# Performance work log

Measured on AMD Instinct MI355X. Metric: run time of the kernel, lower is better.

## Reference

```python
import jax, jax.numpy as jnp
import numpy as np

D = 512
H = 8
HD = D // H  # 64
B = 16
N = 64        # seq_len (variable nodes)
S = N + 1     # new_seq (with CLS)
THRESHOLD = 0.5
LN_EPS = 1e-5


def setup_inputs() -> dict:
    key = jax.random.key(0)
    ks = jax.random.split(key, 12)
    s = 0.02
    return {
        "desc_embeddings": jax.random.normal(ks[0], (B, N, D), jnp.float32),
        "name_value_embeddings": jax.random.normal(ks[1], (B, S, D), jnp.float32),
        "w_gt": jax.random.normal(ks[2], (D, D), jnp.float32) * s,
        "b_gt": jnp.zeros((D,), jnp.float32),
        "topology_bias": jnp.zeros((1,), jnp.float32),
        "w_edge1": jax.random.normal(ks[3], (2 * D, D), jnp.float32) * s,
        "b_edge1": jnp.zeros((D,), jnp.float32),
        "ln_gamma": jnp.ones((D,), jnp.float32),
        "ln_beta": jnp.zeros((D,), jnp.float32),
        "w_edge2": jax.random.normal(ks[4], (D, D), jnp.float32) * s,
        "b_edge2": jnp.zeros((D,), jnp.float32),
        "w_q": jax.random.normal(ks[5], (D, D), jnp.float32) * s,
        "b_q": jnp.zeros((D,), jnp.float32),
        "w_k": jax.random.normal(ks[6], (D, D), jnp.float32) * s,
        "b_k": jnp.zeros((D,), jnp.float32),
        "w_v": jax.random.normal(ks[7], (D, D), jnp.float32) * s,
        "b_v": jnp.zeros((D,), jnp.float32),
        "w_attn": jax.random.normal(ks[8], (3 * HD,), jnp.float32) * s,
        "b_attn": jnp.zeros((1,), jnp.float32),
        "w_out": jax.random.normal(ks[9], (D, D), jnp.float32) * s,
        "b_out": jnp.zeros((D,), jnp.float32),
    }


def _layernorm(x, gamma, beta):
    mu = jnp.mean(x, axis=-1, keepdims=True)
    var = jnp.mean(jnp.square(x - mu), axis=-1, keepdims=True)
    return (x - mu) * jax.lax.rsqrt(var + LN_EPS) * gamma + beta


def reference(desc_embeddings, name_value_embeddings, w_gt, b_gt, topology_bias,
              w_edge1, b_edge1, ln_gamma, ln_beta, w_edge2, b_edge2,
              w_q, b_q, w_k, b_k, w_v, b_v, w_attn, b_attn, w_out, b_out):
    b, s, d = name_value_embeddings.shape
    n = s - 1

    # 1. Global topology (projected desc embeddings, cosine sim, sigmoid)
    de = desc_embeddings @ w_gt + b_gt                                   # [B,N,D]
    de_n = de / jnp.linalg.norm(de, axis=-1, keepdims=True)
    global_sim = jnp.einsum('bnd,bmd->bnm', de_n, de_n)
    gt = jax.nn.sigmoid(global_sim + topology_bias)
    # straight-through threshold (frozen=False)
    hard = (gt > THRESHOLD).astype(gt.dtype)
    gA = hard - jax.lax.stop_gradient(gt) + gt

    # 2. Sample-wise similarity over variable tokens
    var = name_value_embeddings[:, 1:, :]
    var_n = var / jnp.linalg.norm(var, axis=-1, keepdims=True)
    sample_sim = jnp.einsum('bnd,bmd->bnm', var_n, var_n)

    # no self-interaction, then graph-conditioned softmax
    gA = gA * (1.0 - jnp.eye(n, dtype=gt.dtype))[None]
    adjacency = jax.nn.softmax(gA * sample_sim, axis=-1)                 # [B,N,N]

    # 4. Edge attributes [B,S,S,2D] and padded adjacency [B,S,S]
    var_edge = jnp.concatenate([
        jnp.broadcast_to(de[:, :, None, :], (b, n, n, d)),
        jnp.broadcast_to(de[:, None, :, :], (b, n, n, d)),
    ], axis=-1)
    cls_edge = jnp.concatenate([de, de], axis=-1)                        # [B,N,2D]
    edge_attr = jnp.zeros((b, s, s, 2 * d), de.dtype)
    edge_attr = edge_attr.at[:, 1:, 1:].set(var_edge)
    edge_attr = edge_attr.at[:, 0, 1:].set(cls_edge)
    edge_attr = edge_attr.at[:, 1:, 0].set(cls_edge)

    new_adj = jnp.zeros((b, s, s), adjacency.dtype)
    new_adj = new_adj.at[:, 1:, 1:].set(adjacency)
    new_adj = new_adj.at[:, 0, 1:].set(1.0)

    # 5. Attention
    q = (name_value_embeddings @ w_q + b_q).reshape(b, s, H, HD).transpose(0, 2, 1, 3)
    k = (name_value_embeddings @ w_k + b_k).reshape(b, s, H, HD).transpose(0, 2, 1, 3)
    v = (name_value_embeddings @ w_v + b_v).reshape(b, s, H, HD).transpose(0, 2, 1, 3)

    # edge MLP: Linear -> LayerNorm -> ReLU -> Linear
    eu = jax.nn.relu(_layernorm(edge_attr @ w_edge1 + b_edge1, ln_gamma, ln_beta)) @ w_edge2 + b_edge2
    eu = eu.reshape(b, s, s, H, HD)                                      # [B,S,S,H,hd]

    # attn_proj(concat([q_i, k_j, e_ij])) decomposed into three dot products
    wq_a, wk_a, we_a = w_attn[:HD], w_attn[HD:2 * HD], w_attn[2 * HD:]
    score_q = jnp.einsum('bhid,d->bhi', q, wq_a)[:, :, :, None]
    score_k = jnp.einsum('bhjd,d->bhj', k, wk_a)[:, :, None, :]
    # edge features are pre-masked by adjacency; linearity lets us mask the score
    score_e = jnp.einsum('bijhd,d->bhij', eu, we_a) * new_adj[:, None]
    attn = score_q + score_k + score_e + b_attn[0]

    attn = attn + jnp.where(new_adj[:, None] == 0, -1e9, 0.0)
    attn = jax.nn.softmax(attn, axis=-1)                                 # [B,H,S,S]
    # dropout p=0 (eval)

    context = jnp.einsum('bhij,bhjd->bhid', attn, v)
    context = context.transpose(0, 2, 1, 3).reshape(b, s, d)
    output = context @ w_out + b_out
    return output, attn
```

## Files before the change

### kernel.cpp

```cpp
#include <hip/hip_runtime.h>
#include <math.h>


constexpr int kD  = 512;
constexpr int kH  = 8;
constexpr int kHD = 64;
constexpr int kB  = 16;
constexpr int kN  = 64;
constexpr int kS  = 65;

typedef short bf16x8 __attribute__((ext_vector_type(8)));
typedef float f32x4  __attribute__((ext_vector_type(4)));

__device__ __forceinline__ float wsum(float x) {
#pragma unroll
  for (int m = 1; m < 64; m <<= 1) x += __shfl_xor(x, m, 64);
  return x;
}
__device__ __forceinline__ float wmax(float x) {
#pragma unroll
  for (int m = 1; m < 64; m <<= 1) x = fmaxf(x, __shfl_xor(x, m, 64));
  return x;
}
__device__ __forceinline__ float osum(float x) {
  x += __shfl_xor(x, 8, 64);
  x += __shfl_xor(x, 16, 64);
  x += __shfl_xor(x, 32, 64);
  return x;
}

__device__ __forceinline__ unsigned short f2bf(float x) {
  unsigned int u = __builtin_bit_cast(unsigned int, x);
  u += 0x7FFFu + ((u >> 16) & 1u);
  return (unsigned short)(u >> 16);
}
__device__ __forceinline__ float bf2f(unsigned short h) {
  return __builtin_bit_cast(float, ((unsigned int)h) << 16);
}
__device__ __forceinline__ unsigned int pk2(unsigned short a, unsigned short b) {
  return (unsigned int)a | ((unsigned int)b << 16);
}

__global__ __launch_bounds__(256) void conv_w(
    const float* __restrict__ w_q, const float* __restrict__ w_k,
    const float* __restrict__ w_v, const float* __restrict__ w_e1,
    const float* __restrict__ w_o, unsigned short* __restrict__ wt)
{
  __shared__ float T[32][33];
  const int z = blockIdx.z;
  const float* src = (z == 0) ? w_q : (z == 1) ? w_k : (z == 2) ? w_v
                   : (z == 3) ? w_e1 : (z == 4) ? (w_e1 + 262144) : w_o;
  unsigned short* hi = wt + (size_t)z * 524288;
  unsigned short* lo = hi + 262144;
  const int n0 = blockIdx.x * 32, k0 = blockIdx.y * 32;
  const int tx = threadIdx.x & 31, ty0 = threadIdx.x >> 5;
#pragma unroll
  for (int it = 0; it < 4; ++it) {
    const int ky = ty0 + it * 8;
    T[ky][tx] = src[(size_t)(k0 + ky) * kD + n0 + tx];
  }
  __syncthreads();
#pragma unroll
  for (int it = 0; it < 4; ++it) {
    const int ny = ty0 + it * 8;
    const float x = T[tx][ny];
    const unsigned short h = f2bf(x);
    hi[(size_t)(n0 + ny) * kD + k0 + tx] = h;
    lo[(size_t)(n0 + ny) * kD + k0 + tx] = f2bf(x - bf2f(h));
  }
}

__global__ __launch_bounds__(256) void gemm_f32(
    const float* __restrict__ A, const float* __restrict__ W,
    const float* __restrict__ bias, float* __restrict__ C)
{
  __shared__ float Ast[32][65];
  __shared__ float Bs[32][68];
  const int bm = blockIdx.x * 64, bn = blockIdx.y * 64;
  const int tid = threadIdx.x;
  const int ar = tid >> 2, ak = (tid & 3) * 8;
  const int bkr = tid >> 3, bn0 = (tid & 7) * 8;
  const int tx = tid & 15, ty = tid >> 4;
  const float* Ap = A + (size_t)(bm + ar) * kD + ak;
  const float* Wp = W + (size_t)bkr * kD + bn + bn0;

  float4 a0 = *reinterpret_cast<const float4*>(Ap);
  float4 a1 = *reinterpret_cast<const float4*>(Ap + 4);
  float4 b0 = *reinterpret_cast<const float4*>(Wp);
  float4 b1 = *reinterpret_cast<const float4*>(Wp + 4);

  float acc[4][4] = {};
  for (int kt = 0; kt < 16; ++kt) {
    Ast[ak + 0][ar] = a0.x; Ast[ak + 1][ar] = a0.y;
    Ast[ak + 2][ar] = a0.z; Ast[ak + 3][ar] = a0.w;
    Ast[ak + 4][ar] = a1.x; Ast[ak + 5][ar] = a1.y;
    Ast[ak + 6][ar] = a1.z; Ast[ak + 7][ar] = a1.w;
    *reinterpret_cast<float4*>(&Bs[bkr][bn0])     = b0;
    *reinterpret_cast<float4*>(&Bs[bkr][bn0 + 4]) = b1;
    __syncthreads();
    if (kt + 1 < 16) {
      const float* Ap2 = Ap + (kt + 1) * 32;
      const float* Wp2 = Wp + (size_t)(kt + 1) * 32 * kD;
      a0 = *reinterpret_cast<const float4*>(Ap2);
      a1 = *reinterpret_cast<const float4*>(Ap2 + 4);
      b0 = *reinterpret_cast<const float4*>(Wp2);
      b1 = *reinterpret_cast<const float4*>(Wp2 + 4);
    }
#pragma unroll
    for (int kk = 0; kk < 32; ++kk) {
      const float x0 = Ast[kk][ty * 4 + 0];
      const float x1 = Ast[kk][ty * 4 + 1];
      const float x2 = Ast[kk][ty * 4 + 2];
      const float x3 = Ast[kk][ty * 4 + 3];
      const float4 bv = *reinterpret_cast<const float4*>(&Bs[kk][tx * 4]);
      acc[0][0] = fmaf(x0, bv.x, acc[0][0]); acc[0][1] = fmaf(x0, bv.y, acc[0][1]);
      acc[0][2] = fmaf(x0, bv.z, acc[0][2]); acc[0][3] = fmaf(x0, bv.w, acc[0][3]);
      acc[1][0] = fmaf(x1, bv.x, acc[1][0]); acc[1][1] = fmaf(x1, bv.y, acc[1][1]);
      acc[1][2] = fmaf(x1, bv.z, acc[1][2]); acc[1][3] = fmaf(x1, bv.w, acc[1][3]);
      acc[2][0] = fmaf(x2, bv.x, acc[2][0]); acc[2][1] = fmaf(x2, bv.y, acc[2][1]);
      acc[2][2] = fmaf(x2, bv.z, acc[2][2]); acc[2][3] = fmaf(x2, bv.w, acc[2][3]);
      acc[3][0] = fmaf(x3, bv.x, acc[3][0]); acc[3][1] = fmaf(x3, bv.y, acc[3][1]);
      acc[3][2] = fmaf(x3, bv.z, acc[3][2]); acc[3][3] = fmaf(x3, bv.w, acc[3][3]);
    }
    __syncthreads();
  }
#pragma unroll
  for (int i = 0; i < 4; ++i) {
    const int row = bm + ty * 4 + i;
#pragma unroll
    for (int j = 0; j < 4; ++j) {
      const int col = bn + tx * 4 + j;
      C[(size_t)row * kD + col] = acc[i][j] + bias[col];
    }
  }
}

struct MJob { const float* A; const unsigned short* Wh; const unsigned short* Wl;
              const float* bias; float* C; int M; };
struct MJobs { MJob j[3]; };

__global__ __launch_bounds__(256) void gemm_mfma(
    MJobs jobs, int zNorms,
    const float* __restrict__ deN, const float* __restrict__ nvN,
    float* __restrict__ invde, float* __restrict__ invvar)
{
  if ((int)blockIdx.z == zNorms) {
    const int flat = blockIdx.x + gridDim.x * blockIdx.y;
    const int lane = threadIdx.x & 63;
    const int w = threadIdx.x >> 6;
#pragma unroll
    for (int r = 0; r < 4; ++r) {
      const int wid = flat * 16 + w * 4 + r;
      if (wid >= 2 * kB * kN) break;
      const float* row;
      if (wid < kB * kN) {
        row = deN + (size_t)wid * kD;
      } else {
        const int t = wid - kB * kN;
        row = nvN + ((size_t)(t / kN) * kS + 1 + (t % kN)) * kD;
      }
      const float4* r4 = reinterpret_cast<const float4*>(row) + lane * 2;
      const float4 x0 = r4[0], x1 = r4[1];
      float ss = x0.x * x0.x + x0.y * x0.y + x0.z * x0.z + x0.w * x0.w
               + x1.x * x1.x + x1.y * x1.y + x1.z * x1.z + x1.w * x1.w;
      ss = wsum(ss);
      if (lane == 0) {
        const float inv = 1.f / sqrtf(ss);
        if (wid < kB * kN) invde[wid] = inv; else invvar[wid - kB * kN] = inv;
      }
    }
    return;
  }

  const MJob jb = jobs.j[blockIdx.z];
  __shared__ unsigned short Ah[64][40], Al[64][40], Wh[64][40], Wl[64][40];
  const int tid = threadIdx.x;
  const int lane = tid & 63, wv = tid >> 6;
  const int wr = wv >> 1, wc = wv & 1;
  const int bm = blockIdx.x * 64, bn = blockIdx.y * 64;
  const int sr = tid >> 2, sk = (tid & 3) * 8;
  const bool aok = (bm + sr) < jb.M;
  const float* Ap = jb.A + (size_t)(bm + sr) * kD + sk;
  const unsigned short* Whp = jb.Wh + (size_t)(bn + sr) * kD + sk;
  const unsigned short* Wlp = jb.Wl + (size_t)(bn + sr) * kD + sk;

  const f32x4 zero = {0.f, 0.f, 0.f, 0.f};
  f32x4 acc00 = zero, acc01 = zero, acc10 = zero, acc11 = zero;

  for (int k0 = 0; k0 < kD; k0 += 32) {
    float4 a0 = {0.f, 0.f, 0.f, 0.f}, a1 = {0.f, 0.f, 0.f, 0.f};
    if (aok) {
      a0 = *reinterpret_cast<const float4*>(Ap + k0);
      a1 = *reinterpret_cast<const float4*>(Ap + k0 + 4);
    }
    const uint4 wh4 = *reinterpret_cast<const uint4*>(Whp + k0);
    const uint4 wl4 = *reinterpret_cast<const uint4*>(Wlp + k0);
    const float av[8] = {a0.x, a0.y, a0.z, a0.w, a1.x, a1.y, a1.z, a1.w};
    unsigned short h[8], l[8];
#pragma unroll
    for (int e = 0; e < 8; ++e) {
      h[e] = f2bf(av[e]);
      l[e] = f2bf(av[e] - bf2f(h[e]));
    }
    const uint4 hp = { pk2(h[0], h[1]), pk2(h[2], h[3]), pk2(h[4], h[5]), pk2(h[6], h[7]) };
    const uint4 lp = { pk2(l[0], l[1]), pk2(l[2], l[3]), pk2(l[4], l[5]), pk2(l[6], l[7]) };
    *reinterpret_cast<uint4*>(&Ah[sr][sk]) = hp;
    *reinterpret_cast<uint4*>(&Al[sr][sk]) = lp;
    *reinterpret_cast<uint4*>(&Wh[sr][sk]) = wh4;
    *reinterpret_cast<uint4*>(&Wl[sr][sk]) = wl4;
    __syncthreads();

    const int fr = lane & 15, kg = lane >> 4;
#pragma unroll
    for (int fm = 0; fm < 2; ++fm) {
      const int arow = wr * 32 + fm * 16 + fr;
      const bf16x8 amh = *reinterpret_cast<const bf16x8*>(&Ah[arow][kg * 8]);
      const bf16x8 aml = *reinterpret_cast<const bf16x8*>(&Al[arow][kg * 8]);
#pragma unroll
      for (int fn = 0; fn < 2; ++fn) {
        const int wrow = wc * 32 + fn * 16 + fr;
        const bf16x8 bh = *reinterpret_cast<const bf16x8*>(&Wh[wrow][kg * 8]);
        const bf16x8 bl = *reinterpret_cast<const bf16x8*>(&Wl[wrow][kg * 8]);
        f32x4 acc = (fm == 0) ? (fn == 0 ? acc00 : acc01) : (fn == 0 ? acc10 : acc11);
        acc = __builtin_amdgcn_mfma_f32_16x16x32_bf16(amh, bh, acc, 0, 0, 0);
        acc = __builtin_amdgcn_mfma_f32_16x16x32_bf16(amh, bl, acc, 0, 0, 0);
        acc = __builtin_amdgcn_mfma_f32_16x16x32_bf16(aml, bh, acc, 0, 0, 0);
        if (fm == 0) { if (fn == 0) acc00 = acc; else acc01 = acc; }
        else         { if (fn == 0) acc10 = acc; else acc11 = acc; }
      }
    }
    __syncthreads();
  }

  const int rg = lane >> 4, cc = lane & 15;
#pragma unroll
  for (int fm = 0; fm < 2; ++fm) {
#pragma unroll
    for (int fn = 0; fn < 2; ++fn) {
      const f32x4 acc = (fm == 0) ? (fn == 0 ? acc00 : acc01) : (fn == 0 ? acc10 : acc11);
      const int row0 = bm + wr * 32 + fm * 16 + rg * 4;
      const int col  = bn + wc * 32 + fn * 16 + cc;
      const float bb = jb.bias ? jb.bias[col] : 0.f;
#pragma unroll
      for (int e = 0; e < 4; ++e) {
        const int row = row0 + e;
        if (row < jb.M) jb.C[(size_t)row * kD + col] = acc[e] + bb;
      }
    }
  }
}

__global__ __launch_bounds__(512) void graph_prep(
    const float* __restrict__ de, const float* __restrict__ nv,
    const float* __restrict__ invde, const float* __restrict__ invvar,
    const float* __restrict__ topo_p, float* __restrict__ adj,
    const float* __restrict__ q, const float* __restrict__ k,
    const float* __restrict__ w_attn,
    float* __restrict__ sq, float* __restrict__ sk,
    const float* __restrict__ w_edge2, const float* __restrict__ b_edge2,
    float* __restrict__ w2eff, float* __restrict__ b2eff)
{
  const int blk = blockIdx.x;
  if (blk < kB * kN) {
    __shared__ float lg[kN];
    const int b = blk >> 6, i = blk & 63;
    const int w = threadIdx.x >> 6, lane = threadIdx.x & 63;
    const int p = lane & 7, oct = lane >> 3;
    const int j = w * 8 + p;
    const float topo = topo_p[0];
    const float4* di = reinterpret_cast<const float4*>(de + ((size_t)b * kN + i) * kD + oct * 64);
    const float4* dj = reinterpret_cast<const float4*>(de + ((size_t)b * kN + j) * kD + oct * 64);
    const float4* vi = reinterpret_cast<const float4*>(nv + ((size_t)b * kS + 1 + i) * kD + oct * 64);
    const float4* vj = reinterpret_cast<const float4*>(nv + ((size_t)b * kS + 1 + j) * kD + oct * 64);
    float g = 0.f, sv = 0.f;
#pragma unroll
    for (int t = 0; t < 16; ++t) {
      const float4 a = di[t], c = dj[t];
      g += a.x * c.x + a.y * c.y + a.z * c.z + a.w * c.w;
      const float4 x = vi[t], y = vj[t];
      sv += x.x * y.x + x.y * y.y + x.z * y.z + x.w * y.w;
    }
    g = osum(g);
    sv = osum(sv);
    if (oct == 0) {
      const float gs = g * invde[b * kN + i] * invde[b * kN + j] + topo;
      const bool hard = (gs > 0.f) && (j != i);
      lg[j] = hard ? sv * invvar[b * kN + i] * invvar[b * kN + j] : 0.f;
    }
    __syncthreads();
    if (threadIdx.x < 64) {
      const float x = lg[lane];
      const float m = wmax(x);
      const float e = expf(x - m);
      const float s = wsum(e);
      adj[((size_t)b * kN + i) * kN + lane] = e / s;
    }
    return;
  }
  if (blk < kB * kN + 33) {
    const int t = (blk - kB * kN) * 512 + threadIdx.x;
    const int total = kB * kS * kH;
    if (t >= 2 * total) return;
    const int which = (t >= total) ? 1 : 0;
    const int r = which ? t - total : t;
    const int h = r % kH, bs = r / kH;
    const float* src = which ? k : q;
    const float* wa = w_attn + which * kHD;
    const float4* row = reinterpret_cast<const float4*>(src + (size_t)bs * kD + h * kHD);
    const float4* w4 = reinterpret_cast<const float4*>(wa);
    float acc = 0.f;
#pragma unroll
    for (int c = 0; c < kHD / 4; ++c) {
      const float4 a = row[c], w = w4[c];
      acc += a.x * w.x + a.y * w.y + a.z * w.z + a.w * w.w;
    }
    (which ? sk : sq)[r] = acc;
    return;
  }
  {
    const int t = (blk - kB * kN - 33) * 512 + threadIdx.x;
    if (t >= (kD + 1) * kH) return;
    const int c = t >> 3, h = t & 7;
    const float* src = (c < kD) ? (w_edge2 + (size_t)c * kD + h * kHD)
                                : (b_edge2 + h * kHD);
    const float4* s4 = reinterpret_cast<const float4*>(src);
    const float4* wa4 = reinterpret_cast<const float4*>(w_attn + 2 * kHD);
    float acc = 0.f;
#pragma unroll
    for (int u = 0; u < kHD / 4; ++u) {
      const float4 a = s4[u], w = wa4[u];
      acc += a.x * w.x + a.y * w.y + a.z * w.z + a.w * w.w;
    }
    if (c < kD) w2eff[c * kH + h] = acc; else b2eff[h] = acc;
  }
}

__global__ __launch_bounds__(256) void edge_scores(
    const float* __restrict__ Pp, const float* __restrict__ Qq,
    const float* __restrict__ gamma, const float* __restrict__ beta,
    const float* __restrict__ w2eff, const float* __restrict__ b2eff,
    float* __restrict__ es)
{
  const int wid = blockIdx.x * 4 + (threadIdx.x >> 6);
  const int lane = threadIdx.x & 63;
  const int p = lane & 7, oct = lane >> 3;
  const int pair = wid * 8 + p;
  const int b = pair / (kS * kN);
  const int r = pair % (kS * kN);
  const int i = r / kN, jj = r % kN;
  const int prow = b * kN + (i == 0 ? jj : i - 1);
  const int qrow = b * kN + jj;
  const int c0 = oct * 64;
  const float4* Pr = reinterpret_cast<const float4*>(Pp + (size_t)prow * kD + c0);
  const float4* Qr = reinterpret_cast<const float4*>(Qq + (size_t)qrow * kD + c0);

  float4 z4[16];
  float s1 = 0.f, s2 = 0.f;
#pragma unroll
  for (int t = 0; t < 16; ++t) {
    const float4 a = Pr[t], c = Qr[t];
    float4 z;
    z.x = a.x + c.x; z.y = a.y + c.y; z.z = a.z + c.z; z.w = a.w + c.w;
    z4[t] = z;
    s1 += (z.x + z.y) + (z.z + z.w);
    s2 += (z.x * z.x + z.y * z.y) + (z.z * z.z + z.w * z.w);
  }
  s1 = osum(s1);
  s2 = osum(s2);
  const float mu = s1 * (1.f / kD);
  const float var = s2 * (1.f / kD) - mu * mu;
  const float rstd = rsqrtf(var + 1e-5f);
  const float nb = -mu * rstd;

  float acc[8] = {};
#pragma unroll
  for (int t = 0; t < 16; ++t) {
    const float4 g4 = *reinterpret_cast<const float4*>(gamma + c0 + t * 4);
    const float4 b4 = *reinterpret_cast<const float4*>(beta + c0 + t * 4);
    const float zc[4] = { z4[t].x, z4[t].y, z4[t].z, z4[t].w };
    const float gc[4] = { g4.x, g4.y, g4.z, g4.w };
    const float bc[4] = { b4.x, b4.y, b4.z, b4.w };
#pragma unroll
    for (int u = 0; u < 4; ++u) {
      const float zn = fmaf(zc[u], rstd, nb);
      const float eu = fmaxf(fmaf(zn, gc[u], bc[u]), 0.f);
      const float4* w4 = reinterpret_cast<const float4*>(w2eff + (size_t)(c0 + t * 4 + u) * kH);
      const float4 wa = w4[0], wb = w4[1];
      acc[0] = fmaf(eu, wa.x, acc[0]); acc[1] = fmaf(eu, wa.y, acc[1]);
      acc[2] = fmaf(eu, wa.z, acc[2]); acc[3] = fmaf(eu, wa.w, acc[3]);
      acc[4] = fmaf(eu, wb.x, acc[4]); acc[5] = fmaf(eu, wb.y, acc[5]);
      acc[6] = fmaf(eu, wb.z, acc[6]); acc[7] = fmaf(eu, wb.w, acc[7]);
    }
  }
#pragma unroll
  for (int h = 0; h < 8; ++h) acc[h] = osum(acc[h]);
  if (oct == 0) {
    const float4 ba0 = *reinterpret_cast<const float4*>(b2eff);
    const float4 ba1 = *reinterpret_cast<const float4*>(b2eff + 4);
    float* dst = es + (((size_t)b * kS + i) * kS + jj + 1) * kH;
    float4 o0, o1;
    o0.x = acc[0] + ba0.x; o0.y = acc[1] + ba0.y; o0.z = acc[2] + ba0.z; o0.w = acc[3] + ba0.w;
    o1.x = acc[4] + ba1.x; o1.y = acc[5] + ba1.y; o1.z = acc[6] + ba1.z; o1.w = acc[7] + ba1.w;
    reinterpret_cast<float4*>(dst)[0] = o0;
    reinterpret_cast<float4*>(dst)[1] = o1;
  }
}

__global__ __launch_bounds__(576) void attn_ctx(
    const float* __restrict__ sq, const float* __restrict__ sk,
    const float* __restrict__ es, const float* __restrict__ adj,
    const float* __restrict__ v, const float* __restrict__ b_attn,
    float* __restrict__ attn_out, float* __restrict__ ctx)
{
  __shared__ float prob[kH][kS];
  const int bi = blockIdx.x;
  const int b = bi / kS, i = bi % kS;
  const int tid = threadIdx.x;
  const float ba = b_attn[0];
  if (tid < kH * kS) {
    const int h = tid / kS, j = tid % kS;
    float lgv;
    if (j == 0) {
      lgv = -1e30f;
    } else {
      const float a = (i == 0) ? 1.f : adj[((size_t)b * kN + (i - 1)) * kN + (j - 1)];
      lgv = sq[(b * kS + i) * kH + h] + sk[(b * kS + j) * kH + h]
          + es[(((size_t)b * kS + i) * kS + j) * kH + h] * a + ba;
    }
    prob[h][j] = lgv;
  }
  __syncthreads();
  const int w = tid >> 6, lane = tid & 63;
  if (w < kH) {
    const float x = prob[w][lane];
    const float xe = prob[w][64];
    float m = wmax(x);
    m = fmaxf(m, xe);
    const float e = expf(x - m);
    const float ee = expf(xe - m);
    const float s = wsum(e) + ee;
    const float inv = 1.f / s;
    prob[w][lane] = e * inv;
    if (lane == 0) prob[w][64] = ee * inv;
  }
  __syncthreads();
  if (tid < kH * kS) {
    const int h = tid / kS, j = tid % kS;
    attn_out[(((size_t)b * kH + h) * kS + i) * kS + j] = prob[h][j];
  }
  if (tid < kD) {
    const int h = tid >> 6, d = tid & 63;
    const float* vb = v + (size_t)b * kS * kD + h * kHD + d;
    float a0 = 0.f, a1 = 0.f, a2 = 0.f, a3 = 0.f;
#pragma unroll 4
    for (int j = 1; j < kS; j += 4) {
      a0 = fmaf(prob[h][j + 0], vb[(size_t)(j + 0) * kD], a0);
      a1 = fmaf(prob[h][j + 1], vb[(size_t)(j + 1) * kD], a1);
      a2 = fmaf(prob[h][j + 2], vb[(size_t)(j + 2) * kD], a2);
      a3 = fmaf(prob[h][j + 3], vb[(size_t)(j + 3) * kD], a3);
    }
    ctx[((size_t)b * kS + i) * kD + tid] = (a0 + a1) + (a2 + a3);
  }
}

extern "C" void kernel_launch(void* const* d_in, const int* in_sizes, int n_in,
                              void* d_out, int out_size, void* d_ws, size_t ws_size,
                              hipStream_t stream)
{
  const float* desc = (const float*)d_in[0];
  const float* nv   = (const float*)d_in[1];
  const float* w_gt = (const float*)d_in[2];
  const float* b_gt = (const float*)d_in[3];
  const float* topo = (const float*)d_in[4];
  const float* w_e1 = (const float*)d_in[5];
  const float* b_e1 = (const float*)d_in[6];
  const float* ln_g = (const float*)d_in[7];
  const float* ln_b = (const float*)d_in[8];
  const float* w_e2 = (const float*)d_in[9];
  const float* b_e2 = (const float*)d_in[10];
  const float* w_q  = (const float*)d_in[11];
  const float* b_q  = (const float*)d_in[12];
  const float* w_k  = (const float*)d_in[13];
  const float* b_k  = (const float*)d_in[14];
  const float* w_v  = (const float*)d_in[15];
  const float* b_v  = (const float*)d_in[16];
  const float* w_at = (const float*)d_in[17];
  const float* b_at = (const float*)d_in[18];
  const float* w_o  = (const float*)d_in[19];
  const float* b_o  = (const float*)d_in[20];

  float* ws  = (float*)d_ws;
  float* de  = ws;
  float* q   = de  + 524288;
  float* k   = q   + 532480;
  float* v   = k   + 532480;
  float* Pp  = v   + 532480;
  float* Qq  = Pp  + 524288;
  float* adj = Qq  + 524288;
  float* sq  = adj + 65536;
  float* sk  = sq  + 8320;
  float* es  = sk  + 8320;
  float* ctx = es  + 540800;
  float* w2e = ctx + 532480;
  float* b2e = w2e + 4096;
  float* ivd = b2e + 8;
  float* ivv = ivd + 1024;
  unsigned short* wt = (unsigned short*)(ivv + 1024);

  float* out  = (float*)d_out;
  float* attn = out + (size_t)kB * kS * kD;

  conv_w<<<dim3(16, 16, 6), 256, 0, stream>>>(w_q, w_k, w_v, w_e1, w_o, wt);
  gemm_f32<<<dim3(16, 8), 256, 0, stream>>>(desc, w_gt, b_gt, de);
  {
    MJobs jobs;
    jobs.j[0] = { nv, wt + 0u * 524288, wt + 0u * 524288 + 262144, b_q, q, kB * kS };
    jobs.j[1] = { nv, wt + 1u * 524288, wt + 1u * 524288 + 262144, b_k, k, kB * kS };
    jobs.j[2] = { nv, wt + 2u * 524288, wt + 2u * 524288 + 262144, b_v, v, kB * kS };
    gemm_mfma<<<dim3(17, 8, 3), 256, 0, stream>>>(jobs, -1, nullptr, nullptr, nullptr, nullptr);
  }
  {
    MJobs jobs;
    jobs.j[0] = { de, wt + 3u * 524288, wt + 3u * 524288 + 262144, b_e1,   Pp, kB * kN };
    jobs.j[1] = { de, wt + 4u * 524288, wt + 4u * 524288 + 262144, nullptr, Qq, kB * kN };
    jobs.j[2] = jobs.j[0];
    gemm_mfma<<<dim3(16, 8, 3), 256, 0, stream>>>(jobs, 2, de, nv, ivd, ivv);
  }
  graph_prep<<<1066, 512, 0, stream>>>(de, nv, ivd, ivv, topo, adj,
                                       q, k, w_at, sq, sk,
                                       w_e2, b_e2, w2e, b2e);
  edge_scores<<<2080, 256, 0, stream>>>(Pp, Qq, ln_g, ln_b, w2e, b2e, es);
  attn_ctx<<<kB * kS, 576, 0, stream>>>(sq, sk, es, adj, v, b_at, attn, ctx);
  {
    MJobs jobs;
    jobs.j[0] = { ctx, wt + 5u * 524288, wt + 5u * 524288 + 262144, b_o, out, kB * kS };
    jobs.j[1] = jobs.j[0]; jobs.j[2] = jobs.j[0];
    gemm_mfma<<<dim3(17, 8, 1), 256, 0, stream>>>(jobs, -1, nullptr, nullptr, nullptr, nullptr);
  }
}
```

Measured before the change: 315.5 us.

## Move edge-score projection to split-bf16 MFMA and fold desc GEMM into batched MFMA

The edge_scores kernel now computes the LayerNorm+ReLU edge activations per 16-pair tile and projects them onto the 8 per-head attention weights with bf16 MFMA. It uses a hi/lo split (three MFMAs) to keep accuracy near fp32, replacing the scalar FMA loop and cross-lane reductions. graph_prep now writes the collapsed w_edge2·w_attn matrix as a zero-padded transposed bf16 hi/lo pair. The scalar fp32 desc projection GEMM is removed: w_gt is converted alongside the other weights and the projection runs as a fourth job in the batched MFMA launch. The trade-offs are half the MFMA columns wasted on padding and a small precision change from the bf16 splitting.

```diff
diff --git a/kernel.cpp b/kernel.cpp
--- a/kernel.cpp
+++ b/kernel.cpp
@@ -44,12 +44,14 @@
 __global__ __launch_bounds__(256) void conv_w(
     const float* __restrict__ w_q, const float* __restrict__ w_k,
     const float* __restrict__ w_v, const float* __restrict__ w_e1,
-    const float* __restrict__ w_o, unsigned short* __restrict__ wt)
+    const float* __restrict__ w_o, const float* __restrict__ w_gt,
+    unsigned short* __restrict__ wt)
 {
   __shared__ float T[32][33];
   const int z = blockIdx.z;
   const float* src = (z == 0) ? w_q : (z == 1) ? w_k : (z == 2) ? w_v
-                   : (z == 3) ? w_e1 : (z == 4) ? (w_e1 + 262144) : w_o;
+                   : (z == 3) ? w_e1 : (z == 4) ? (w_e1 + 262144)
+                   : (z == 5) ? w_o : w_gt;
   unsigned short* hi = wt + (size_t)z * 524288;
   unsigned short* lo = hi + 262144;
   const int n0 = blockIdx.x * 32, k0 = blockIdx.y * 32;
@@ -70,74 +72,9 @@
   }
 }
 
-__global__ __launch_bounds__(256) void gemm_f32(
-    const float* __restrict__ A, const float* __restrict__ W,
-    const float* __restrict__ bias, float* __restrict__ C)
-{
-  __shared__ float Ast[32][65];
-  __shared__ float Bs[32][68];
-  const int bm = blockIdx.x * 64, bn = blockIdx.y * 64;
-  const int tid = threadIdx.x;
-  const int ar = tid >> 2, ak = (tid & 3) * 8;
-  const int bkr = tid >> 3, bn0 = (tid & 7) * 8;
-  const int tx = tid & 15, ty = tid >> 4;
-  const float* Ap = A + (size_t)(bm + ar) * kD + ak;
-  const float* Wp = W + (size_t)bkr * kD + bn + bn0;
-
-  float4 a0 = *reinterpret_cast<const float4*>(Ap);
-  float4 a1 = *reinterpret_cast<const float4*>(Ap + 4);
-  float4 b0 = *reinterpret_cast<const float4*>(Wp);
-  float4 b1 = *reinterpret_cast<const float4*>(Wp + 4);
-
-  float acc[4][4] = {};
-  for (int kt = 0; kt < 16; ++kt) {
-    Ast[ak + 0][ar] = a0.x; Ast[ak + 1][ar] = a0.y;
-    Ast[ak + 2][ar] = a0.z; Ast[ak + 3][ar] = a0.w;
-    Ast[ak + 4][ar] = a1.x; Ast[ak + 5][ar] = a1.y;
-    Ast[ak + 6][ar] = a1.z; Ast[ak + 7][ar] = a1.w;
-    *reinterpret_cast<float4*>(&Bs[bkr][bn0])     = b0;
-    *reinterpret_cast<float4*>(&Bs[bkr][bn0 + 4]) = b1;
-    __syncthreads();
-    if (kt + 1 < 16) {
-      const float* Ap2 = Ap + (kt + 1) * 32;
-      const float* Wp2 = Wp + (size_t)(kt + 1) * 32 * kD;
-      a0 = *reinterpret_cast<const float4*>(Ap2);
-      a1 = *reinterpret_cast<const float4*>(Ap2 + 4);
-      b0 = *reinterpret_cast<const float4*>(Wp2);
-      b1 = *reinterpret_cast<const float4*>(Wp2 + 4);
-    }
-#pragma unroll
-    for (int kk = 0; kk < 32; ++kk) {
-      const float x0 = Ast[kk][ty * 4 + 0];
-      const float x1 = Ast[kk][ty * 4 + 1];
-      const float x2 = Ast[kk][ty * 4 + 2];
-      const float x3 = Ast[kk][ty * 4 + 3];
-      const float4 bv = *reinterpret_cast<const float4*>(&Bs[kk][tx * 4]);
-      acc[0][0] = fmaf(x0, bv.x, acc[0][0]); acc[0][1] = fmaf(x0, bv.y, acc[0][1]);
-      acc[0][2] = fmaf(x0, bv.z, acc[0][2]); acc[0][3] = fmaf(x0, bv.w, acc[0][3]);
-      acc[1][0] = fmaf(x1, bv.x, acc[1][0]); acc[1][1] = fmaf(x1, bv.y, acc[1][1]);
-      acc[1][2] = fmaf(x1, bv.z, acc[1][2]); acc[1][3] = fmaf(x1, bv.w, acc[1][3]);
-      acc[2][0] = fmaf(x2, bv.x, acc[2][0]); acc[2][1] = fmaf(x2, bv.y, acc[2][1]);
-      acc[2][2] = fmaf(x2, bv.z, acc[2][2]); acc[2][3] = fmaf(x2, bv.w, acc[2][3]);
-      acc[3][0] = fmaf(x3, bv.x, acc[3][0]); acc[3][1] = fmaf(x3, bv.y, acc[3][1]);
-      acc[3][2] = fmaf(x3, bv.z, acc[3][2]); acc[3][3] = fmaf(x3, bv.w, acc[3][3]);
-    }
-    __syncthreads();
-  }
-#pragma unroll
-  for (int i = 0; i < 4; ++i) {
-    const int row = bm + ty * 4 + i;
-#pragma unroll
-    for (int j = 0; j < 4; ++j) {
-      const int col = bn + tx * 4 + j;
-      C[(size_t)row * kD + col] = acc[i][j] + bias[col];
-    }
-  }
-}
-
 struct MJob { const float* A; const unsigned short* Wh; const unsigned short* Wl;
               const float* bias; float* C; int M; };
-struct MJobs { MJob j[3]; };
+struct MJobs { MJob j[4]; };
 
 __global__ __launch_bounds__(256) void gemm_mfma(
     MJobs jobs, int zNorms,
@@ -258,7 +195,8 @@
     const float* __restrict__ w_attn,
     float* __restrict__ sq, float* __restrict__ sk,
     const float* __restrict__ w_edge2, const float* __restrict__ b_edge2,
-    float* __restrict__ w2eff, float* __restrict__ b2eff)
+    unsigned short* __restrict__ w2ph, unsigned short* __restrict__ w2pl,
+    float* __restrict__ b2eff)
 {
   const int blk = blockIdx.x;
   if (blk < kB * kN) {
@@ -318,91 +256,122 @@
     return;
   }
   {
-    const int t = (blk - kB * kN - 33) * 512 + threadIdx.x;
-    if (t >= (kD + 1) * kH) return;
-    const int c = t >> 3, h = t & 7;
-    const float* src = (c < kD) ? (w_edge2 + (size_t)c * kD + h * kHD)
-                                : (b_edge2 + h * kHD);
-    const float4* s4 = reinterpret_cast<const float4*>(src);
+    const int rel = blk - (kB * kN + 33);
     const float4* wa4 = reinterpret_cast<const float4*>(w_attn + 2 * kHD);
-    float acc = 0.f;
-#pragma unroll
-    for (int u = 0; u < kHD / 4; ++u) {
-      const float4 a = s4[u], w = wa4[u];
-      acc += a.x * w.x + a.y * w.y + a.z * w.z + a.w * w.w;
-    }
-    if (c < kD) w2eff[c * kH + h] = acc; else b2eff[h] = acc;
+    if (rel < 8) {
+      const int t = rel * 512 + threadIdx.x;
+      const int c = t >> 3, h = t & 7;
+      const float4* s4 = reinterpret_cast<const float4*>(w_edge2 + (size_t)c * kD + h * kHD);
+      float acc = 0.f;
+#pragma unroll
+      for (int u = 0; u < kHD / 4; ++u) {
+        const float4 a = s4[u], w = wa4[u];
+        acc += a.x * w.x + a.y * w.y + a.z * w.z + a.w * w.w;
+      }
+      const unsigned short hi = f2bf(acc);
+      w2ph[h * kD + c] = hi;
+      w2pl[h * kD + c] = f2bf(acc - bf2f(hi));
+    } else {
+      if (threadIdx.x < kH) {
+        const int h = threadIdx.x;
+        float acc = 0.f;
+        for (int d = 0; d < kHD; ++d)
+          acc += b_edge2[h * kHD + d] * w_attn[2 * kHD + d];
+        b2eff[h] = acc;
+      }
+      for (int u = threadIdx.x; u < 8 * kD; u += 512) {
+        w2ph[8 * kD + u] = 0;
+        w2pl[8 * kD + u] = 0;
+      }
+    }
   }
 }
 
 __global__ __launch_bounds__(256) void edge_scores(
     const float* __restrict__ Pp, const float* __restrict__ Qq,
     const float* __restrict__ gamma, const float* __restrict__ beta,
-    const float* __restrict__ w2eff, const float* __restrict__ b2eff,
-    float* __restrict__ es)
+    const unsigned short* __restrict__ w2ph, const unsigned short* __restrict__ w2pl,
+    const float* __restrict__ b2eff, float* __restrict__ es)
 {
-  const int wid = blockIdx.x * 4 + (threadIdx.x >> 6);
+  const int g = blockIdx.x * 4 + (threadIdx.x >> 6);
   const int lane = threadIdx.x & 63;
-  const int p = lane & 7, oct = lane >> 3;
-  const int pair = wid * 8 + p;
-  const int b = pair / (kS * kN);
-  const int r = pair % (kS * kN);
-  const int i = r / kN, jj = r % kN;
-  const int prow = b * kN + (i == 0 ? jj : i - 1);
+  const int m = lane & 15, kg = lane >> 4;
+  const int base = g * 16;
+  const int b = base / (kS * kN);
+  const int r0 = base % (kS * kN);
+  const int i = r0 / kN, j0 = r0 % kN;
+  const int jj = j0 + m;
   const int qrow = b * kN + jj;
-  const int c0 = oct * 64;
-  const float4* Pr = reinterpret_cast<const float4*>(Pp + (size_t)prow * kD + c0);
-  const float4* Qr = reinterpret_cast<const float4*>(Qq + (size_t)qrow * kD + c0);
-
-  float4 z4[16];
+  const int prow = (i == 0) ? qrow : (b * kN + i - 1);
+  const float* Pr = Pp + (size_t)prow * kD;
+  const float* Qr = Qq + (size_t)qrow * kD;
+
   float s1 = 0.f, s2 = 0.f;
-#pragma unroll
-  for (int t = 0; t < 16; ++t) {
-    const float4 a = Pr[t], c = Qr[t];
-    float4 z;
-    z.x = a.x + c.x; z.y = a.y + c.y; z.z = a.z + c.z; z.w = a.w + c.w;
-    z4[t] = z;
-    s1 += (z.x + z.y) + (z.z + z.w);
-    s2 += (z.x * z.x + z.y * z.y) + (z.z * z.z + z.w * z.w);
-  }
-  s1 = osum(s1);
-  s2 = osum(s2);
+#pragma unroll 4
+  for (int s = 0; s < 16; ++s) {
+    const int c = s * 32 + kg * 8;
+    const float4 pa = *reinterpret_cast<const float4*>(Pr + c);
+    const float4 pb = *reinterpret_cast<const float4*>(Pr + c + 4);
+    const float4 qa = *reinterpret_cast<const float4*>(Qr + c);
+    const float4 qb = *reinterpret_cast<const float4*>(Qr + c + 4);
+    const float z0 = pa.x + qa.x, z1 = pa.y + qa.y, z2 = pa.z + qa.z, z3 = pa.w + qa.w;
+    const float z4 = pb.x + qb.x, z5 = pb.y + qb.y, z6 = pb.z + qb.z, z7 = pb.w + qb.w;
+    s1 += ((z0 + z1) + (z2 + z3)) + ((z4 + z5) + (z6 + z7));
+    s2 += ((z0 * z0 + z1 * z1) + (z2 * z2 + z3 * z3))
+        + ((z4 * z4 + z5 * z5) + (z6 * z6 + z7 * z7));
+  }
+  s1 += __shfl_xor(s1, 16, 64); s1 += __shfl_xor(s1, 32, 64);
+  s2 += __shfl_xor(s2, 16, 64); s2 += __shfl_xor(s2, 32, 64);
   const float mu = s1 * (1.f / kD);
   const float var = s2 * (1.f / kD) - mu * mu;
   const float rstd = rsqrtf(var + 1e-5f);
   const float nb = -mu * rstd;
 
-  float acc[8] = {};
-#pragma unroll
-  for (int t = 0; t < 16; ++t) {
-    const float4 g4 = *reinterpret_cast<const float4*>(gamma + c0 + t * 4);
-    const float4 b4 = *reinterpret_cast<const float4*>(beta + c0 + t * 4);
-    const float zc[4] = { z4[t].x, z4[t].y, z4[t].z, z4[t].w };
-    const float gc[4] = { g4.x, g4.y, g4.z, g4.w };
-    const float bc[4] = { b4.x, b4.y, b4.z, b4.w };
-#pragma unroll
-    for (int u = 0; u < 4; ++u) {
-      const float zn = fmaf(zc[u], rstd, nb);
-      const float eu = fmaxf(fmaf(zn, gc[u], bc[u]), 0.f);
-      const float4* w4 = reinterpret_cast<const float4*>(w2eff + (size_t)(c0 + t * 4 + u) * kH);
-      const float4 wa = w4[0], wb = w4[1];
-      acc[0] = fmaf(eu, wa.x, acc[0]); acc[1] = fmaf(eu, wa.y, acc[1]);
-      acc[2] = fmaf(eu, wa.z, acc[2]); acc[3] = fmaf(eu, wa.w, acc[3]);
-      acc[4] = fmaf(eu, wb.x, acc[4]); acc[5] = fmaf(eu, wb.y, acc[5]);
-      acc[6] = fmaf(eu, wb.z, acc[6]); acc[7] = fmaf(eu, wb.w, acc[7]);
-    }
-  }
-#pragma unroll
-  for (int h = 0; h < 8; ++h) acc[h] = osum(acc[h]);
-  if (oct == 0) {
-    const float4 ba0 = *reinterpret_cast<const float4*>(b2eff);
-    const float4 ba1 = *reinterpret_cast<const float4*>(b2eff + 4);
-    float* dst = es + (((size_t)b * kS + i) * kS + jj + 1) * kH;
-    float4 o0, o1;
-    o0.x = acc[0] + ba0.x; o0.y = acc[1] + ba0.y; o0.z = acc[2] + ba0.z; o0.w = acc[3] + ba0.w;
-    o1.x = acc[4] + ba1.x; o1.y = acc[5] + ba1.y; o1.z = acc[6] + ba1.z; o1.w = acc[7] + ba1.w;
-    reinterpret_cast<float4*>(dst)[0] = o0;
-    reinterpret_cast<float4*>(dst)[1] = o1;
+  const f32x4 zero = {0.f, 0.f, 0.f, 0.f};
+  f32x4 accA = zero, accB = zero, accC = zero;
+#pragma unroll 4
+  for (int s = 0; s < 16; ++s) {
+    const int c = s * 32 + kg * 8;
+    const float4 pa = *reinterpret_cast<const float4*>(Pr + c);
+    const float4 pb = *reinterpret_cast<const float4*>(Pr + c + 4);
+    const float4 qa = *reinterpret_cast<const float4*>(Qr + c);
+    const float4 qb = *reinterpret_cast<const float4*>(Qr + c + 4);
+    const float4 ga = *reinterpret_cast<const float4*>(gamma + c);
+    const float4 gb = *reinterpret_cast<const float4*>(gamma + c + 4);
+    const float4 ba = *reinterpret_cast<const float4*>(beta + c);
+    const float4 bb = *reinterpret_cast<const float4*>(beta + c + 4);
+    const float zv[8] = { pa.x + qa.x, pa.y + qa.y, pa.z + qa.z, pa.w + qa.w,
+                          pb.x + qb.x, pb.y + qb.y, pb.z + qb.z, pb.w + qb.w };
+    const float gv[8] = { ga.x, ga.y, ga.z, ga.w, gb.x, gb.y, gb.z, gb.w };
+    const float bv[8] = { ba.x, ba.y, ba.z, ba.w, bb.x, bb.y, bb.z, bb.w };
+    unsigned short h8[8], l8[8];
+#pragma unroll
+    for (int e = 0; e < 8; ++e) {
+      const float zn = fmaf(zv[e], rstd, nb);
+      const float eu = fmaxf(fmaf(zn, gv[e], bv[e]), 0.f);
+      h8[e] = f2bf(eu);
+      l8[e] = f2bf(eu - bf2f(h8[e]));
+    }
+    const uint4 hp = { pk2(h8[0], h8[1]), pk2(h8[2], h8[3]), pk2(h8[4], h8[5]), pk2(h8[6], h8[7]) };
+    const uint4 lp = { pk2(l8[0], l8[1]), pk2(l8[2], l8[3]), pk2(l8[4], l8[5]), pk2(l8[6], l8[7]) };
+    const bf16x8 Af_h = __builtin_bit_cast(bf16x8, hp);
+    const bf16x8 Af_l = __builtin_bit_cast(bf16x8, lp);
+    const bf16x8 Bh = *reinterpret_cast<const bf16x8*>(w2ph + (size_t)m * kD + c);
+    const bf16x8 Bl = *reinterpret_cast<const bf16x8*>(w2pl + (size_t)m * kD + c);
+    accA = __builtin_amdgcn_mfma_f32_16x16x32_bf16(Af_h, Bh, accA, 0, 0, 0);
+    accB = __builtin_amdgcn_mfma_f32_16x16x32_bf16(Af_h, Bl, accB, 0, 0, 0);
+    accC = __builtin_amdgcn_mfma_f32_16x16x32_bf16(Af_l, Bh, accC, 0, 0, 0);
+  }
+
+  const int n = lane & 15;
+  if (n < kH) {
+    const float be = b2eff[n];
+#pragma unroll
+    for (int e = 0; e < 4; ++e) {
+      const int mp = kg * 4 + e;
+      es[(((size_t)b * kS + i) * kS + (j0 + mp + 1)) * kH + n]
+          = (accA[e] + accB[e]) + accC[e] + be;
+    }
   }
 }
 
@@ -501,40 +470,41 @@
   float* sk  = sq  + 8320;
   float* es  = sk  + 8320;
   float* ctx = es  + 540800;
-  float* w2e = ctx + 532480;
-  float* b2e = w2e + 4096;
+  float* b2e = ctx + 532480;
   float* ivd = b2e + 8;
   float* ivv = ivd + 1024;
-  unsigned short* wt = (unsigned short*)(ivv + 1024);
+  unsigned short* wt   = (unsigned short*)(ivv + 1024);
+  unsigned short* w2ph = wt + 7u * 524288;
+  unsigned short* w2pl = w2ph + 8192;
 
   float* out  = (float*)d_out;
   float* attn = out + (size_t)kB * kS * kD;
 
-  conv_w<<<dim3(16, 16, 6), 256, 0, stream>>>(w_q, w_k, w_v, w_e1, w_o, wt);
-  gemm_f32<<<dim3(16, 8), 256, 0, stream>>>(desc, w_gt, b_gt, de);
+  conv_w<<<dim3(16, 16, 7), 256, 0, stream>>>(w_q, w_k, w_v, w_e1, w_o, w_gt, wt);
   {
     MJobs jobs;
-    jobs.j[0] = { nv, wt + 0u * 524288, wt + 0u * 524288 + 262144, b_q, q, kB * kS };
-    jobs.j[1] = { nv, wt + 1u * 524288, wt + 1u * 524288 + 262144, b_k, k, kB * kS };
-    jobs.j[2] = { nv, wt + 2u * 524288, wt + 2u * 524288 + 262144, b_v, v, kB * kS };
-    gemm_mfma<<<dim3(17, 8, 3), 256, 0, stream>>>(jobs, -1, nullptr, nullptr, nullptr, nullptr);
+    jobs.j[0] = { desc, wt + 6u * 524288, wt + 6u * 524288 + 262144, b_gt, de, kB * kN };
+    jobs.j[1] = { nv,   wt + 0u * 524288, wt + 0u * 524288 + 262144, b_q,  q,  kB * kS };
+    jobs.j[2] = { nv,   wt + 1u * 524288, wt + 1u * 524288 + 262144, b_k,  k,  kB * kS };
+    jobs.j[3] = { nv,   wt + 2u * 524288, wt + 2u * 524288 + 262144, b_v,  v,  kB * kS };
+    gemm_mfma<<<dim3(17, 8, 4), 256, 0, stream>>>(jobs, -1, nullptr, nullptr, nullptr, nullptr);
   }
   {
     MJobs jobs;
     jobs.j[0] = { de, wt + 3u * 524288, wt + 3u * 524288 + 262144, b_e1,   Pp, kB * kN };
     jobs.j[1] = { de, wt + 4u * 524288, wt + 4u * 524288 + 262144, nullptr, Qq, kB * kN };
-    jobs.j[2] = jobs.j[0];
+    jobs.j[2] = jobs.j[0]; jobs.j[3] = jobs.j[0];
     gemm_mfma<<<dim3(16, 8, 3), 256, 0, stream>>>(jobs, 2, de, nv, ivd, ivv);
   }
   graph_prep<<<1066, 512, 0, stream>>>(de, nv, ivd, ivv, topo, adj,
                                        q, k, w_at, sq, sk,
-                                       w_e2, b_e2, w2e, b2e);
-  edge_scores<<<2080, 256, 0, stream>>>(Pp, Qq, ln_g, ln_b, w2e, b2e, es);
+                                       w_e2, b_e2, w2ph, w2pl, b2e);
+  edge_scores<<<1040, 256, 0, stream>>>(Pp, Qq, ln_g, ln_b, w2ph, w2pl, b2e, es);
   attn_ctx<<<kB * kS, 576, 0, stream>>>(sq, sk, es, adj, v, b_at, attn, ctx);
   {
     MJobs jobs;
     jobs.j[0] = { ctx, wt + 5u * 524288, wt + 5u * 524288 + 262144, b_o, out, kB * kS };
-    jobs.j[1] = jobs.j[0]; jobs.j[2] = jobs.j[0];
+    jobs.j[1] = jobs.j[0]; jobs.j[2] = jobs.j[0]; jobs.j[3] = jobs.j[0];
     gemm_mfma<<<dim3(17, 8, 1), 256, 0, stream>>>(jobs, -1, nullptr, nullptr, nullptr, nullptr);
   }
 }
```

After: 300.6 us. -4.7%, faster.
